# Performance work log

Hardware: AMD Instinct MI355X
Metric: run time of the kernel (lower is better)

## Reference

```python
import jax, jax.numpy as jnp
import numpy as np

B = 32768
L = 1024            # harmonics length (from 1365 = L + L//3)
HID = 256
OUT = 1024


def setup_inputs() -> dict:
    key = jax.random.key(0)
    k1, k2, k3 = jax.random.split(key, 3)
    x = jax.random.normal(k1, (B, 1, L), dtype=jnp.float32)
    W1 = jax.random.normal(k2, (HID, 1365), dtype=jnp.float32) * 0.02
    b1 = jnp.zeros((HID,), dtype=jnp.float32)
    W2 = jax.random.normal(k3, (OUT, HID), dtype=jnp.float32) * 0.02
    b2 = jnp.zeros((OUT,), dtype=jnp.float32)
    return {"x": x, "W1": W1, "b1": b1, "W2": W2, "b2": b2}


def reference(x, W1, b1, W2, b2):
    # backbone is identity; squeeze channel dim -> harmonics_pred [B, L]
    h = x[:, 0, :]
    # multi-scale average pooling (method='average'), vectorized over batch
    s1 = h                                               # scale 1: [B, 1024]
    s2 = h[:, : (L // 2) * 2].reshape(-1, L // 2, 2).mean(axis=-1)   # [B, 512]
    s3 = h[:, : (L // 3) * 3].reshape(-1, L // 3, 3).mean(axis=-1)   # [B, 341]
    m = L // 3                                           # min_len = 341
    summed = s1[:, :m] + s2[:, :m] + s3                  # [B, 341]
    feat = jnp.concatenate([h, summed], axis=1)          # [B, 1365]
    # fund_head MLP (dropout inactive in eval)
    hid = jax.nn.relu(feat @ W1.T + b1)                  # [B, 256]
    fund = hid @ W2.T + b2                               # [B, 1024]
    return fund[:, None, :], h
```

## Files before the change

### kernel.cpp

```cpp
#include <hip/hip_runtime.h>
#include <stdint.h>
#include <stddef.h>

typedef __attribute__((ext_vector_type(8))) short short8;
typedef __attribute__((ext_vector_type(4))) float floatx4;

#define MFMA_BF16(A, B, C) __builtin_amdgcn_mfma_f32_16x16x32_bf16((A), (B), (C), 0, 0, 0)

static constexpr int NB   = 32768;
static constexpr int LV   = 1024;
static constexpr int HIDV = 256;
static constexpr int OUTV = 1024;
static constexpr size_t HOFF = (size_t)NB * OUTV;

__device__ __forceinline__ short f2bf(float f) {
  union { float f; uint32_t u; } c; c.f = f;
  uint32_t u = c.u;
  u += 0x7fffu + ((u >> 16) & 1u);
  return (short)(u >> 16);
}

__global__ __launch_bounds__(256) void wconv1eff(const float* __restrict__ W1,
                                                 short* __restrict__ w1bf) {
  int idx = blockIdx.x * 256 + threadIdx.x;
  int n = idx >> 10;
  int k = idx & 1023;
  const float* r = W1 + (size_t)n * 1365;
  float v = r[k];
  if (k < 341)  v += r[1024 + k];
  if (k < 682)  v += 0.5f * r[1024 + (k >> 1)];
  if (k < 1023) v += (1.f / 3.f) * r[1024 + k / 3];
  w1bf[idx] = f2bf(v);
}

__global__ __launch_bounds__(256) void wconv2(const float* __restrict__ W2,
                                              short* __restrict__ w2bf) {
  int idx = blockIdx.x * 256 + threadIdx.x;
  w2bf[idx] = f2bf(W2[idx]);
}

__global__ __launch_bounds__(512, 4) void gemm_fused(
    const float* __restrict__ x,
    const short* __restrict__ w1bf, const short* __restrict__ w2bf,
    const float* __restrict__ b1, const float* __restrict__ b2,
    float* __restrict__ out) {
  __shared__ __align__(16) short Abuf[2][64 * 72];
  __shared__ __align__(16) short Hbuf[64 * 264];

  const int tid  = threadIdx.x;
  const int wave = tid >> 6;
  const int lane = tid & 63;
  const int l15  = lane & 15;
  const int quad = lane >> 4;
  const int row0 = blockIdx.x * 64;

  const int srow = tid >> 3;
  const int sseg = tid & 7;

  float4 xa, xb;
  const floatx4 fzero = {0.f, 0.f, 0.f, 0.f};

  const float4* xrow = reinterpret_cast<const float4*>(x + (size_t)(row0 + srow) * LV);
  float4* hrow = reinterpret_cast<float4*>(out + HOFF + (size_t)(row0 + srow) * LV);

  auto loadA = [&](int ck) {
    xa = xrow[ck * 16 + 2 * sseg];
    xb = xrow[ck * 16 + 2 * sseg + 1];
  };
  auto writeA = [&](int buf, int ck) {
    short8 p;
    p[0] = f2bf(xa.x); p[1] = f2bf(xa.y); p[2] = f2bf(xa.z); p[3] = f2bf(xa.w);
    p[4] = f2bf(xb.x); p[5] = f2bf(xb.y); p[6] = f2bf(xb.z); p[7] = f2bf(xb.w);
    *reinterpret_cast<short8*>(&Abuf[buf][srow * 72 + sseg * 8]) = p;
    hrow[ck * 16 + 2 * sseg]     = xa;
    hrow[ck * 16 + 2 * sseg + 1] = xb;
  };

  short8 Breg[4], Bnxt[4];
  auto loadB1 = [&](int ck, short8* dst) {
    #pragma unroll
    for (int ks = 0; ks < 2; ++ks)
      #pragma unroll
      for (int ns = 0; ns < 2; ++ns)
        dst[ks * 2 + ns] = *reinterpret_cast<const short8*>(
            w1bf + (size_t)(wave * 32 + ns * 16 + l15) * LV + ck * 64 + ks * 32 + quad * 8);
  };

  floatx4 acc1[4][2];
  #pragma unroll
  for (int ms = 0; ms < 4; ++ms)
    #pragma unroll
    for (int ns = 0; ns < 2; ++ns)
      acc1[ms][ns] = fzero;

  loadA(0);
  loadB1(0, Breg);

  #pragma unroll 1
  for (int ck = 0; ck < 16; ++ck) {
    const int buf = ck & 1;
    writeA(buf, ck);
    if (ck < 15) { loadA(ck + 1); loadB1(ck + 1, Bnxt); }
    __syncthreads();
    #pragma unroll
    for (int ks = 0; ks < 2; ++ks) {
      short8 afr[4];
      #pragma unroll
      for (int ms = 0; ms < 4; ++ms)
        afr[ms] = *reinterpret_cast<const short8*>(
            &Abuf[buf][(ms * 16 + l15) * 72 + ks * 32 + quad * 8]);
      #pragma unroll
      for (int ms = 0; ms < 4; ++ms)
        #pragma unroll
        for (int ns = 0; ns < 2; ++ns)
          acc1[ms][ns] = MFMA_BF16(afr[ms], Breg[ks * 2 + ns], acc1[ms][ns]);
    }
    #pragma unroll
    for (int i = 0; i < 4; ++i) Breg[i] = Bnxt[i];
  }

  #pragma unroll
  for (int ms = 0; ms < 4; ++ms) {
    #pragma unroll
    for (int ns = 0; ns < 2; ++ns) {
      const int n = wave * 32 + ns * 16 + l15;
      const float bias = b1[n];
      #pragma unroll
      for (int r = 0; r < 4; ++r) {
        const int m = ms * 16 + quad * 4 + r;
        float v = acc1[ms][ns][r] + bias;
        Hbuf[m * 264 + n] = f2bf(v > 0.f ? v : 0.f);
      }
    }
  }
  __syncthreads();

  short8 B2[2], B2n[2];
  auto loadB2 = [&](int q, int kc, short8* dst) {
    #pragma unroll
    for (int ns = 0; ns < 2; ++ns)
      dst[ns] = *reinterpret_cast<const short8*>(
          w2bf + (size_t)(q * 256 + wave * 32 + ns * 16 + l15) * HIDV + kc * 32 + quad * 8);
  };

  #pragma unroll 1
  for (int q = 0; q < 4; ++q) {
    floatx4 acc2[4][2];
    #pragma unroll
    for (int ms = 0; ms < 4; ++ms)
      #pragma unroll
      for (int ns = 0; ns < 2; ++ns)
        acc2[ms][ns] = fzero;
    loadB2(q, 0, B2);
    #pragma unroll 1
    for (int kc = 0; kc < 8; ++kc) {
      short8 afr[4];
      #pragma unroll
      for (int ms = 0; ms < 4; ++ms)
        afr[ms] = *reinterpret_cast<const short8*>(
            &Hbuf[(ms * 16 + l15) * 264 + kc * 32 + quad * 8]);
      if (kc < 7) loadB2(q, kc + 1, B2n);
      #pragma unroll
      for (int ms = 0; ms < 4; ++ms)
        #pragma unroll
        for (int ns = 0; ns < 2; ++ns)
          acc2[ms][ns] = MFMA_BF16(afr[ms], B2[ns], acc2[ms][ns]);
      #pragma unroll
      for (int i = 0; i < 2; ++i) B2[i] = B2n[i];
    }
    #pragma unroll
    for (int ms = 0; ms < 4; ++ms) {
      #pragma unroll
      for (int ns = 0; ns < 2; ++ns) {
        const int o = q * 256 + wave * 32 + ns * 16 + l15;
        const float bias = b2[o];
        #pragma unroll
        for (int r = 0; r < 4; ++r) {
          const int m = ms * 16 + quad * 4 + r;
          out[(size_t)(row0 + m) * OUTV + o] = acc2[ms][ns][r] + bias;
        }
      }
    }
  }
}

extern "C" void kernel_launch(void* const* d_in, const int* in_sizes, int n_in,
                              void* d_out, int out_size, void* d_ws, size_t ws_size,
                              hipStream_t stream) {
  const float* x  = (const float*)d_in[0];
  const float* W1 = (const float*)d_in[1];
  const float* b1 = (const float*)d_in[2];
  const float* W2 = (const float*)d_in[3];
  const float* b2 = (const float*)d_in[4];
  float* out = (float*)d_out;

  char* ws = (char*)d_ws;
  short* w1bf = (short*)(ws);
  short* w2bf = (short*)(ws + 524288);

  hipLaunchKernelGGL(wconv1eff, dim3(1024), dim3(256), 0, stream, W1, w1bf);
  hipLaunchKernelGGL(wconv2,    dim3(1024), dim3(256), 0, stream, W2, w2bf);
  hipLaunchKernelGGL(gemm_fused, dim3(NB / 64), dim3(512), 0, stream,
                     x, w1bf, w2bf, b1, b2, out);
}
```

Before: 424.9 us.

## Merge weight prep kernels, use LDS-only barrier, and prefetch W2 across quarters

Combines the two weight-conversion kernels into one launch to save a kernel launch. In the main GEMM loop, replaces __syncthreads with an lgkmcnt-only wait plus s_barrier, so pending global loads and stores no longer drain at the barrier. It also moves the h-copy global stores after the barrier. The W2 fragment prefetch now crosses quarter boundaries so the first load of each quarter is overlapped. This relies on manual waitcnt correctness, with some risk if the compiler reorders memory operations.

```diff
diff --git a/kernel.cpp b/kernel.cpp
--- a/kernel.cpp
+++ b/kernel.cpp
@@ -20,23 +20,24 @@
   return (short)(u >> 16);
 }
 
-__global__ __launch_bounds__(256) void wconv1eff(const float* __restrict__ W1,
-                                                 short* __restrict__ w1bf) {
+__global__ __launch_bounds__(256) void wprep(const float* __restrict__ W1,
+                                             const float* __restrict__ W2,
+                                             short* __restrict__ w1bf,
+                                             short* __restrict__ w2bf) {
   int idx = blockIdx.x * 256 + threadIdx.x;
-  int n = idx >> 10;
-  int k = idx & 1023;
-  const float* r = W1 + (size_t)n * 1365;
-  float v = r[k];
-  if (k < 341)  v += r[1024 + k];
-  if (k < 682)  v += 0.5f * r[1024 + (k >> 1)];
-  if (k < 1023) v += (1.f / 3.f) * r[1024 + k / 3];
-  w1bf[idx] = f2bf(v);
-}
-
-__global__ __launch_bounds__(256) void wconv2(const float* __restrict__ W2,
-                                              short* __restrict__ w2bf) {
-  int idx = blockIdx.x * 256 + threadIdx.x;
-  w2bf[idx] = f2bf(W2[idx]);
+  if (idx < 256 * 1024) {
+    int n = idx >> 10;
+    int k = idx & 1023;
+    const float* r = W1 + (size_t)n * 1365;
+    float v = r[k];
+    if (k < 341)  v += r[1024 + k];
+    if (k < 682)  v += 0.5f * r[1024 + (k >> 1)];
+    if (k < 1023) v += (1.f / 3.f) * r[1024 + k / 3];
+    w1bf[idx] = f2bf(v);
+  } else {
+    int j = idx - 256 * 1024;
+    w2bf[j] = f2bf(W2[j]);
+  }
 }
 
 __global__ __launch_bounds__(512, 4) void gemm_fused(
@@ -67,11 +68,13 @@
     xa = xrow[ck * 16 + 2 * sseg];
     xb = xrow[ck * 16 + 2 * sseg + 1];
   };
-  auto writeA = [&](int buf, int ck) {
+  auto writeA = [&](int buf) {
     short8 p;
     p[0] = f2bf(xa.x); p[1] = f2bf(xa.y); p[2] = f2bf(xa.z); p[3] = f2bf(xa.w);
     p[4] = f2bf(xb.x); p[5] = f2bf(xb.y); p[6] = f2bf(xb.z); p[7] = f2bf(xb.w);
     *reinterpret_cast<short8*>(&Abuf[buf][srow * 72 + sseg * 8]) = p;
+  };
+  auto storeH = [&](int ck) {
     hrow[ck * 16 + 2 * sseg]     = xa;
     hrow[ck * 16 + 2 * sseg + 1] = xb;
   };
@@ -99,9 +102,12 @@
   #pragma unroll 1
   for (int ck = 0; ck < 16; ++ck) {
     const int buf = ck & 1;
-    writeA(buf, ck);
+    writeA(buf);
+    asm volatile("s_waitcnt lgkmcnt(0)" ::: "memory");
+    __builtin_amdgcn_s_barrier();
+    asm volatile("" ::: "memory");
+    storeH(ck);
     if (ck < 15) { loadA(ck + 1); loadB1(ck + 1, Bnxt); }
-    __syncthreads();
     #pragma unroll
     for (int ks = 0; ks < 2; ++ks) {
       short8 afr[4];
@@ -133,7 +139,9 @@
       }
     }
   }
-  __syncthreads();
+  asm volatile("s_waitcnt lgkmcnt(0)" ::: "memory");
+  __builtin_amdgcn_s_barrier();
+  asm volatile("" ::: "memory");
 
   short8 B2[2], B2n[2];
   auto loadB2 = [&](int q, int kc, short8* dst) {
@@ -143,6 +151,7 @@
           w2bf + (size_t)(q * 256 + wave * 32 + ns * 16 + l15) * HIDV + kc * 32 + quad * 8);
   };
 
+  loadB2(0, 0, B2);
   #pragma unroll 1
   for (int q = 0; q < 4; ++q) {
     floatx4 acc2[4][2];
@@ -151,7 +160,6 @@
       #pragma unroll
       for (int ns = 0; ns < 2; ++ns)
         acc2[ms][ns] = fzero;
-    loadB2(q, 0, B2);
     #pragma unroll 1
     for (int kc = 0; kc < 8; ++kc) {
       short8 afr[4];
@@ -159,7 +167,8 @@
       for (int ms = 0; ms < 4; ++ms)
         afr[ms] = *reinterpret_cast<const short8*>(
             &Hbuf[(ms * 16 + l15) * 264 + kc * 32 + quad * 8]);
-      if (kc < 7) loadB2(q, kc + 1, B2n);
+      const int t = q * 8 + kc + 1;
+      if (t < 32) loadB2(t >> 3, t & 7, B2n);
       #pragma unroll
       for (int ms = 0; ms < 4; ++ms)
         #pragma unroll
@@ -198,8 +207,7 @@
   short* w1bf = (short*)(ws);
   short* w2bf = (short*)(ws + 524288);
 
-  hipLaunchKernelGGL(wconv1eff, dim3(1024), dim3(256), 0, stream, W1, w1bf);
-  hipLaunchKernelGGL(wconv2,    dim3(1024), dim3(256), 0, stream, W2, w2bf);
+  hipLaunchKernelGGL(wprep, dim3(2048), dim3(256), 0, stream, W1, W2, w1bf, w2bf);
   hipLaunchKernelGGL(gemm_fused, dim3(NB / 64), dim3(512), 0, stream,
                      x, w1bf, w2bf, b1, b2, out);
 }
```

After: 416.2 us. 1.02x faster.
